# Optimization experiments

Measured on AMD Instinct MI355X. Metric: run time of the kernel, lower is better.

The kernel has to match this reference:

```python
import jax, jax.numpy as jnp
import numpy as np

DIM = 128      # size_in
SIGN = 4       # number of leading outputs negated
CONST = 0.618  # additive constant in Linear_v5
BATCH = 4096


def setup_inputs() -> dict:
    key = jax.random.key(0)
    k0, k1, k2, k3, k4 = jax.random.split(key, 5)
    s1 = 1.0 / np.sqrt(DIM)
    s2 = 1.0 / np.sqrt(2 * DIM)
    return {
        "t": 0,
        "input_": jax.random.normal(k0, (BATCH, 2 * DIM), dtype=jnp.float32),
        "W1": jax.random.uniform(k1, (2 * DIM, DIM), jnp.float32, -s1, s1),
        "b1": jax.random.uniform(k2, (2 * DIM,), jnp.float32, -s1, s1),
        "W2": jax.random.uniform(k3, (DIM, 2 * DIM), jnp.float32, -s2, s2),
        "b2": jax.random.uniform(k4, (DIM,), jnp.float32, -s2, s2),
    }


def reference(t, input_, W1, b1, W2, b2):
    x = input_[:, :DIM]   # [B, D]
    v = input_[:, DIM:]   # [B, D]
    dtype = x.dtype
    # sign vector: first SIGN outputs of g are negated (applied after sigmoid+const)
    sgn = jnp.where(jnp.arange(DIM) < SIGN, -1.0, 1.0).astype(dtype)  # [D]

    h = x @ W1.T + b1                      # [B, 2D]
    a = jax.nn.relu(h)
    s = jax.nn.sigmoid(a @ W2.T + b2)      # [B, D]
    g = sgn * (s + CONST)                  # [B, D]

    # Analytic batch Jacobian J[b,i,j] = d g_i / d x_j
    # = sgn_i * s_i(1-s_i) * sum_k W2[i,k] * 1[h_bk>0] * W1[k,j]
    mask = (h > 0).astype(dtype)           # [B, 2D]
    Jcore = jnp.einsum('ik,bk,kj->bij', W2, mask, W1)   # [B, D, D]
    J = (sgn * (s * (1.0 - s)))[:, :, None] * Jcore      # [B, D, D]

    g_inv = 1.0 / g                        # [B, D]
    conn1 = -J * g_inv[:, None, :]         # [B, i, j] * g_inv_j
    conn2 = J * g_inv[:, :, None]          # [B, i, j] * g_inv_i

    dv_vec = v[:, :, None] * v[:, None, :]               # [B, i, j] = v_i v_j
    vtemp1 = jnp.sum((v * v)[:, :, None] * conn1, axis=1)  # sum_i v_i^2 conn1[b,i,j]
    vtemp2 = jnp.einsum('bji,bji->bj', dv_vec, conn2)
    vtemp3 = jnp.einsum('bij,bji->bj', dv_vec, conn2)
    dv = vtemp1 + vtemp2 + vtemp3          # [B, D]

    return jnp.concatenate([v, dv], axis=1)  # [B, 2D]
```

## Files before the change

### kernel.cpp

```cpp
#include <hip/hip_runtime.h>
#include <math.h>

#define DIM    128
#define DIM2   256
#define NSIGN  4
#define CCONST 0.618f
#define MB     16
#define NTHR   1024

typedef short bf16x8 __attribute__((ext_vector_type(8)));
typedef float f32x4  __attribute__((ext_vector_type(4)));

#define MFMA(a,b,c) __builtin_amdgcn_mfma_f32_16x16x32_bf16((a),(b),(c),0,0,0)

union BU { uint4 q; bf16x8 b; };

__device__ __forceinline__ unsigned short f2bf(float f) {
    unsigned u = __float_as_uint(f);
    u += 0x7fffu + ((u >> 16) & 1u);
    return (unsigned short)(u >> 16);
}
__device__ __forceinline__ float bf2f(unsigned short h) {
    return __uint_as_float(((unsigned)h) << 16);
}
__device__ __forceinline__ bf16x8 frag16(const unsigned short* p) {
    BU u; u.q = *(const uint4*)p; return u.b;
}

__global__ void prep_pack(const float* __restrict__ W1, const float* __restrict__ W2,
                          unsigned short* __restrict__ pk) {
    int tid  = blockIdx.x * 256 + threadIdx.x;
    int m    = tid >> 12;
    int f    = tid & 4095;
    int lane = f & 63;
    int tkt  = f >> 6;
    int r0   = ((tkt & ((m == 0 || m == 2) ? 3 : 7)) * 32) + ((lane >> 4) << 3);
    int nt   = tkt / ((m == 0 || m == 2) ? 4 : 8);
    int c    = nt * 16 + (lane & 15);

    union { uint4 q; unsigned short u[8]; } H, L;
    #pragma unroll
    for (int e = 0; e < 8; ++e) {
        int r = r0 + e;
        float v;
        if      (m == 0) v = W1[c * DIM  + r];
        else if (m == 1) v = W2[c * DIM2 + r];
        else if (m == 2) v = W2[r * DIM2 + c];
        else             v = W1[r * DIM  + c];
        unsigned short hb = f2bf(v);
        H.u[e] = hb;
        L.u[e] = f2bf(v - bf2f(hb));
    }
    size_t base = (size_t)m * 65536 + (size_t)(tkt * 64 + lane) * 8;
    *(uint4*)(pk + base) = H.q;
    if (m == 0) *(uint4*)(pk + base + 32768) = L.q;
}

__global__ __launch_bounds__(NTHR)
void fused_connection(const float* __restrict__ input_,
                      const float* __restrict__ b1,
                      const float* __restrict__ b2,
                      const unsigned short* __restrict__ pk,
                      float* __restrict__ out) {
    __shared__ __align__(16) float          vv [MB][132];
    __shared__ __align__(16) unsigned short xbH[MB][136];
    __shared__ __align__(16) unsigned short xbL[MB][136];
    __shared__ __align__(16) unsigned short vbH[MB][136];
    __shared__ __align__(16) unsigned short aH [MB][264];
    __shared__ __align__(16) unsigned short mwH[MB][264];
    __shared__ __align__(16) unsigned short vcH[MB][136];

    const int t    = threadIdx.x;
    const int lane = t & 63;
    const int w    = t >> 6;
    const int b0   = blockIdx.x * MB;
    const int arow = lane & 15;
    const int kg   = (lane >> 4) << 3;
    const int rbase = (lane >> 4) << 2;

    uint4 b1hq[4], b1lq[4];
    #pragma unroll
    for (int kt = 0; kt < 4; ++kt) {
        const unsigned short* bp = pk + (size_t)(((w * 4 + kt) * 64 + lane) * 8);
        b1hq[kt] = *(const uint4*)bp;
        b1lq[kt] = *(const uint4*)(bp + 32768);
    }
    const float b1v = b1[w * 16 + arow];
    float b2v = 0.f;
    if (w < 8) b2v = b2[w * 16 + arow];

    {
        int prow = t >> 6;
        int pc   = (t & 63) * 4;
        const float4 f = *(const float4*)(input_ + (size_t)(b0 + prow) * DIM2 + pc);
        float fa[4] = {f.x, f.y, f.z, f.w};
        if (pc < DIM) {
            union { unsigned short u[4]; ushort4 q; } H, L;
            #pragma unroll
            for (int e = 0; e < 4; ++e) {
                unsigned short hb = f2bf(fa[e]);
                H.u[e] = hb;
                L.u[e] = f2bf(fa[e] - bf2f(hb));
            }
            *(ushort4*)&xbH[prow][pc] = H.q;
            *(ushort4*)&xbL[prow][pc] = L.q;
        } else {
            int c = pc - DIM;
            *(float4*)&vv[prow][c] = f;
            union { unsigned short u[4]; ushort4 q; } H;
            #pragma unroll
            for (int e = 0; e < 4; ++e) H.u[e] = f2bf(fa[e]);
            *(ushort4*)&vbH[prow][c] = H.q;
            *(float4*)(out + (size_t)(b0 + prow) * DIM2 + c) = f;
        }
    }
    __syncthreads();

    {
        f32x4 ha = {0.f, 0.f, 0.f, 0.f};
        f32x4 wa = {0.f, 0.f, 0.f, 0.f};
        #pragma unroll
        for (int kt = 0; kt < 4; ++kt) {
            int k0 = kt * 32 + kg;
            bf16x8 xH = frag16(&xbH[arow][k0]);
            bf16x8 xL = frag16(&xbL[arow][k0]);
            bf16x8 vH = frag16(&vbH[arow][k0]);
            BU bh, bl;
            bh.q = b1hq[kt];
            bl.q = b1lq[kt];
            ha = MFMA(xH, bh.b, ha);
            ha = MFMA(xH, bl.b, ha);
            ha = MFMA(xL, bh.b, ha);
            wa = MFMA(vH, bh.b, wa);
        }
        int col = w * 16 + arow;
        #pragma unroll
        for (int reg = 0; reg < 4; ++reg) {
            int row = rbase + reg;
            float hv = ha[reg] + b1v;
            bool  mk = hv > 0.f;
            aH[row][col]  = f2bf(mk ? hv : 0.f);
            mwH[row][col] = f2bf(mk ? wa[reg] : 0.f);
        }
    }
    __syncthreads();

    float sreg[4];
    f32x4 t2a = {0.f, 0.f, 0.f, 0.f};
    if (w < 8) {
        const unsigned short* p1 = pk + 65536;
        f32x4 za = {0.f, 0.f, 0.f, 0.f};
        #pragma unroll
        for (int kt = 0; kt < 8; ++kt) {
            int k0 = kt * 32 + kg;
            bf16x8 af = frag16(&aH[arow][k0]);
            bf16x8 mf = frag16(&mwH[arow][k0]);
            BU bh; bh.q = *(const uint4*)(p1 + (size_t)((w * 8 + kt) * 64 + lane) * 8);
            za  = MFMA(af, bh.b, za);
            t2a = MFMA(mf, bh.b, t2a);
        }
        int   ci   = w * 16 + arow;
        float sg_i = (ci < NSIGN) ? -1.f : 1.f;
        #pragma unroll
        for (int reg = 0; reg < 4; ++reg) {
            int row = rbase + reg;
            float z = za[reg] + b2v;
            float s = 1.f / (1.f + __expf(-z));
            sreg[reg] = s;
            float vvl = vv[row][ci];
            vcH[row][ci] = f2bf(vvl * vvl * sg_i * s * (1.f - s));
        }
    }
    __syncthreads();

    {
        const unsigned short* p2 = pk + 2 * 65536;
        f32x4 ua = {0.f, 0.f, 0.f, 0.f};
        #pragma unroll
        for (int kt = 0; kt < 4; ++kt) {
            bf16x8 cH = frag16(&vcH[arow][kt * 32 + kg]);
            BU bh; bh.q = *(const uint4*)(p2 + (size_t)(((w * 4 + kt) * 64 + lane) * 8));
            ua = MFMA(cH, bh.b, ua);
        }
        int ck = w * 16 + arow;
        #pragma unroll
        for (int reg = 0; reg < 4; ++reg) {
            int row = rbase + reg;
            bool mk = aH[row][ck] != 0;
            mwH[row][ck] = f2bf(mk ? ua[reg] : 0.f);
        }
    }
    __syncthreads();

    if (w < 8) {
        const unsigned short* p3 = pk + 3 * 65536;
        f32x4 t1a = {0.f, 0.f, 0.f, 0.f};
        #pragma unroll
        for (int kt = 0; kt < 8; ++kt) {
            bf16x8 mf = frag16(&mwH[arow][kt * 32 + kg]);
            BU bh; bh.q = *(const uint4*)(p3 + (size_t)((w * 8 + kt) * 64 + lane) * 8);
            t1a = MFMA(mf, bh.b, t1a);
        }
        int   cj   = w * 16 + arow;
        float sg_j = (cj < NSIGN) ? -1.f : 1.f;
        #pragma unroll
        for (int reg = 0; reg < 4; ++reg) {
            int row = rbase + reg;
            float s  = sreg[reg];
            float cv = sg_j * s * (1.f - s);
            float gi = 1.f / (sg_j * (s + CCONST));
            float vvl = vv[row][cj];
            float dv = fmaf(-gi, t1a[reg], 2.f * vvl * gi * cv * t2a[reg]);
            out[(size_t)(b0 + row) * DIM2 + DIM + cj] = dv;
        }
    }
}

extern "C" void kernel_launch(void* const* d_in, const int* in_sizes, int n_in,
                              void* d_out, int out_size, void* d_ws, size_t ws_size,
                              hipStream_t stream) {
    const float* input_ = (const float*)d_in[1];
    const float* W1 = (const float*)d_in[2];
    const float* b1 = (const float*)d_in[3];
    const float* W2 = (const float*)d_in[4];
    const float* b2 = (const float*)d_in[5];
    float* out = (float*)d_out;
    unsigned short* pk = (unsigned short*)d_ws;

    const int batch = in_sizes[1] / DIM2;

    prep_pack<<<64, 256, 0, stream>>>(W1, W2, pk);
    fused_connection<<<batch / MB, NTHR, 0, stream>>>(input_, b1, b2, pk, out);
}
```

Measured before the change: 18.00 us.

## Halve batch tile to 8 rows and remap waves to keep all busy

Reduces rows per block from 16 to 8 and threads from 1024 to 512, so twice as many blocks are launched. The A fragment rows are duplicated (lane&7), which wastes half of each MFMA, and only lanes <32 store results. Every wave now handles two N-tiles in stages 1 and 3 and one tile in stages 2 and 4, so no waves sit idle. Weight fragments for the next stage are prefetched into registers before each barrier. The cost is twice the MFMA work per row and more register pressure under the 4-blocks-per-CU launch bound.

```diff
diff --git a/kernel.cpp b/kernel.cpp
--- a/kernel.cpp
+++ b/kernel.cpp
@@ -5,8 +5,8 @@
 #define DIM2   256
 #define NSIGN  4
 #define CCONST 0.618f
-#define MB     16
-#define NTHR   1024
+#define MB     8
+#define NTHR   512
 
 typedef short bf16x8 __attribute__((ext_vector_type(8)));
 typedef float f32x4  __attribute__((ext_vector_type(4)));
@@ -56,7 +56,7 @@
     if (m == 0) *(uint4*)(pk + base + 32768) = L.q;
 }
 
-__global__ __launch_bounds__(NTHR)
+__global__ __launch_bounds__(NTHR, 4)
 void fused_connection(const float* __restrict__ input_,
                       const float* __restrict__ b1,
                       const float* __restrict__ b2,
@@ -74,20 +74,21 @@
     const int lane = t & 63;
     const int w    = t >> 6;
     const int b0   = blockIdx.x * MB;
-    const int arow = lane & 15;
+    const int arow = lane & 7;
+    const int ncol = lane & 15;
     const int kg   = (lane >> 4) << 3;
     const int rbase = (lane >> 4) << 2;
-
-    uint4 b1hq[4], b1lq[4];
+    const bool storer = (lane < 32);
+
+    uint4 b1hq[2][4];
     #pragma unroll
-    for (int kt = 0; kt < 4; ++kt) {
-        const unsigned short* bp = pk + (size_t)(((w * 4 + kt) * 64 + lane) * 8);
-        b1hq[kt] = *(const uint4*)bp;
-        b1lq[kt] = *(const uint4*)(bp + 32768);
-    }
-    const float b1v = b1[w * 16 + arow];
-    float b2v = 0.f;
-    if (w < 8) b2v = b2[w * 16 + arow];
+    for (int nt2 = 0; nt2 < 2; ++nt2)
+        #pragma unroll
+        for (int kt = 0; kt < 4; ++kt)
+            b1hq[nt2][kt] = *(const uint4*)(pk + (size_t)((((w * 2 + nt2) * 4 + kt) * 64 + lane) * 8));
+    const float b1v0 = b1[(w * 2 + 0) * 16 + ncol];
+    const float b1v1 = b1[(w * 2 + 1) * 16 + ncol];
+    const float b2v  = b2[w * 16 + ncol];
 
     {
         int prow = t >> 6;
@@ -116,102 +117,138 @@
     }
     __syncthreads();
 
-    {
-        f32x4 ha = {0.f, 0.f, 0.f, 0.f};
-        f32x4 wa = {0.f, 0.f, 0.f, 0.f};
-        #pragma unroll
-        for (int kt = 0; kt < 4; ++kt) {
-            int k0 = kt * 32 + kg;
-            bf16x8 xH = frag16(&xbH[arow][k0]);
-            bf16x8 xL = frag16(&xbL[arow][k0]);
-            bf16x8 vH = frag16(&vbH[arow][k0]);
-            BU bh, bl;
-            bh.q = b1hq[kt];
-            bl.q = b1lq[kt];
-            ha = MFMA(xH, bh.b, ha);
-            ha = MFMA(xH, bl.b, ha);
-            ha = MFMA(xL, bh.b, ha);
-            wa = MFMA(vH, bh.b, wa);
-        }
-        int col = w * 16 + arow;
-        #pragma unroll
-        for (int reg = 0; reg < 4; ++reg) {
-            int row = rbase + reg;
-            float hv = ha[reg] + b1v;
-            bool  mk = hv > 0.f;
-            aH[row][col]  = f2bf(mk ? hv : 0.f);
-            mwH[row][col] = f2bf(mk ? wa[reg] : 0.f);
+    uint4 b2q[8];
+    {
+        const unsigned short* p1 = pk + 65536;
+        #pragma unroll
+        for (int kt = 0; kt < 8; ++kt)
+            b2q[kt] = *(const uint4*)(p1 + (size_t)((w * 8 + kt) * 64 + lane) * 8);
+
+        #pragma unroll
+        for (int nt2 = 0; nt2 < 2; ++nt2) {
+            f32x4 ha = {0.f, 0.f, 0.f, 0.f};
+            f32x4 wa = {0.f, 0.f, 0.f, 0.f};
+            #pragma unroll
+            for (int kt = 0; kt < 4; ++kt) {
+                int k0 = kt * 32 + kg;
+                bf16x8 xH = frag16(&xbH[arow][k0]);
+                bf16x8 xL = frag16(&xbL[arow][k0]);
+                bf16x8 vH = frag16(&vbH[arow][k0]);
+                const unsigned short* blp =
+                    pk + (size_t)((((w * 2 + nt2) * 4 + kt) * 64 + lane) * 8) + 32768;
+                BU bh; bh.q = b1hq[nt2][kt];
+                BU bl; bl.q = *(const uint4*)blp;
+                ha = MFMA(xH, bh.b, ha);
+                ha = MFMA(xH, bl.b, ha);
+                ha = MFMA(xL, bh.b, ha);
+                wa = MFMA(vH, bh.b, wa);
+            }
+            if (storer) {
+                int col  = (w * 2 + nt2) * 16 + ncol;
+                float bias = nt2 ? b1v1 : b1v0;
+                #pragma unroll
+                for (int reg = 0; reg < 4; ++reg) {
+                    int row = rbase + reg;
+                    float hv = ha[reg] + bias;
+                    bool  mk = hv > 0.f;
+                    aH[row][col]  = f2bf(mk ? hv : 0.f);
+                    mwH[row][col] = f2bf(mk ? wa[reg] : 0.f);
+                }
+            }
         }
     }
     __syncthreads();
 
     float sreg[4];
     f32x4 t2a = {0.f, 0.f, 0.f, 0.f};
-    if (w < 8) {
-        const unsigned short* p1 = pk + 65536;
+    uint4 b3q[2][4];
+    {
+        const unsigned short* p2 = pk + 2 * 65536;
+        #pragma unroll
+        for (int nt2 = 0; nt2 < 2; ++nt2)
+            #pragma unroll
+            for (int kt = 0; kt < 4; ++kt)
+                b3q[nt2][kt] = *(const uint4*)(p2 + (size_t)((((w * 2 + nt2) * 4 + kt) * 64 + lane) * 8));
+
         f32x4 za = {0.f, 0.f, 0.f, 0.f};
         #pragma unroll
         for (int kt = 0; kt < 8; ++kt) {
             int k0 = kt * 32 + kg;
             bf16x8 af = frag16(&aH[arow][k0]);
             bf16x8 mf = frag16(&mwH[arow][k0]);
-            BU bh; bh.q = *(const uint4*)(p1 + (size_t)((w * 8 + kt) * 64 + lane) * 8);
+            BU bh; bh.q = b2q[kt];
             za  = MFMA(af, bh.b, za);
             t2a = MFMA(mf, bh.b, t2a);
         }
-        int   ci   = w * 16 + arow;
-        float sg_i = (ci < NSIGN) ? -1.f : 1.f;
-        #pragma unroll
-        for (int reg = 0; reg < 4; ++reg) {
-            int row = rbase + reg;
-            float z = za[reg] + b2v;
-            float s = 1.f / (1.f + __expf(-z));
-            sreg[reg] = s;
-            float vvl = vv[row][ci];
-            vcH[row][ci] = f2bf(vvl * vvl * sg_i * s * (1.f - s));
-        }
-    }
-    __syncthreads();
-
-    {
-        const unsigned short* p2 = pk + 2 * 65536;
-        f32x4 ua = {0.f, 0.f, 0.f, 0.f};
-        #pragma unroll
-        for (int kt = 0; kt < 4; ++kt) {
-            bf16x8 cH = frag16(&vcH[arow][kt * 32 + kg]);
-            BU bh; bh.q = *(const uint4*)(p2 + (size_t)(((w * 4 + kt) * 64 + lane) * 8));
-            ua = MFMA(cH, bh.b, ua);
-        }
-        int ck = w * 16 + arow;
-        #pragma unroll
-        for (int reg = 0; reg < 4; ++reg) {
-            int row = rbase + reg;
-            bool mk = aH[row][ck] != 0;
-            mwH[row][ck] = f2bf(mk ? ua[reg] : 0.f);
-        }
-    }
-    __syncthreads();
-
-    if (w < 8) {
+        if (storer) {
+            int   ci   = w * 16 + ncol;
+            float sg_i = (ci < NSIGN) ? -1.f : 1.f;
+            #pragma unroll
+            for (int reg = 0; reg < 4; ++reg) {
+                int row = rbase + reg;
+                float z = za[reg] + b2v;
+                float s = 1.f / (1.f + __expf(-z));
+                sreg[reg] = s;
+                float vvl = vv[row][ci];
+                vcH[row][ci] = f2bf(vvl * vvl * sg_i * s * (1.f - s));
+            }
+        }
+    }
+    __syncthreads();
+
+    uint4 b4q[8];
+    {
         const unsigned short* p3 = pk + 3 * 65536;
+        #pragma unroll
+        for (int kt = 0; kt < 8; ++kt)
+            b4q[kt] = *(const uint4*)(p3 + (size_t)((w * 8 + kt) * 64 + lane) * 8);
+
+        bf16x8 cH[4];
+        #pragma unroll
+        for (int kt = 0; kt < 4; ++kt)
+            cH[kt] = frag16(&vcH[arow][kt * 32 + kg]);
+        #pragma unroll
+        for (int nt2 = 0; nt2 < 2; ++nt2) {
+            f32x4 ua = {0.f, 0.f, 0.f, 0.f};
+            #pragma unroll
+            for (int kt = 0; kt < 4; ++kt) {
+                BU bh; bh.q = b3q[nt2][kt];
+                ua = MFMA(cH[kt], bh.b, ua);
+            }
+            if (storer) {
+                int ck = (w * 2 + nt2) * 16 + ncol;
+                #pragma unroll
+                for (int reg = 0; reg < 4; ++reg) {
+                    int row = rbase + reg;
+                    bool mk = aH[row][ck] != 0;
+                    mwH[row][ck] = f2bf(mk ? ua[reg] : 0.f);
+                }
+            }
+        }
+    }
+    __syncthreads();
+
+    {
         f32x4 t1a = {0.f, 0.f, 0.f, 0.f};
         #pragma unroll
         for (int kt = 0; kt < 8; ++kt) {
             bf16x8 mf = frag16(&mwH[arow][kt * 32 + kg]);
-            BU bh; bh.q = *(const uint4*)(p3 + (size_t)((w * 8 + kt) * 64 + lane) * 8);
+            BU bh; bh.q = b4q[kt];
             t1a = MFMA(mf, bh.b, t1a);
         }
-        int   cj   = w * 16 + arow;
-        float sg_j = (cj < NSIGN) ? -1.f : 1.f;
-        #pragma unroll
-        for (int reg = 0; reg < 4; ++reg) {
-            int row = rbase + reg;
-            float s  = sreg[reg];
-            float cv = sg_j * s * (1.f - s);
-            float gi = 1.f / (sg_j * (s + CCONST));
-            float vvl = vv[row][cj];
-            float dv = fmaf(-gi, t1a[reg], 2.f * vvl * gi * cv * t2a[reg]);
-            out[(size_t)(b0 + row) * DIM2 + DIM + cj] = dv;
+        if (storer) {
+            int   cj   = w * 16 + ncol;
+            float sg_j = (cj < NSIGN) ? -1.f : 1.f;
+            #pragma unroll
+            for (int reg = 0; reg < 4; ++reg) {
+                int row = rbase + reg;
+                float s  = sreg[reg];
+                float cv = sg_j * s * (1.f - s);
+                float gi = 1.f / (sg_j * (s + CCONST));
+                float vvl = vv[row][cj];
+                float dv = fmaf(-gi, t1a[reg], 2.f * vvl * gi * cv * t2a[reg]);
+                out[(size_t)(b0 + row) * DIM2 + DIM + cj] = dv;
+            }
         }
     }
 }
```

After: 19.49 us. 1.08x slower.
